# Kernel optimization log

Measured on AMD Instinct MI355X. Metric: run time of the kernel, lower is better.

Reference implementation:

```python
import jax, jax.numpy as jnp
import numpy as np

MASK_VALUE = 0.0
MAX_PATCHES = 7
MASK_MODES = ['courtain', 'center', 'border', 'patches']
B, C, H, W = 64, 3, 512, 512


def _build_mask(rng):
    # Faithful host-side replication of RandomMask's per-sample mask generation.
    mask = np.zeros((B, 1, H, W), dtype=np.float32)
    for i in range(B):
        mode = rng.choice(MASK_MODES)
        if mode == 'courtain':
            edge = rng.choice(['left', 'right', 'top', 'bottom'])
            pct = rng.uniform(0.1, 0.7)
            if edge == 'left':
                mask[i, :, :int(pct * H)] = 1
            elif edge == 'right':
                mask[i, :, int(pct * H):] = 1
            elif edge == 'top':
                mask[i, :, :, :int(pct * W)] = 1
            else:  # bottom
                mask[i, :, :, int(pct * W):] = 1
        elif mode in ('center', 'border'):
            pad_w = int(rng.uniform(0.1, 0.5) * H)
            pad_h = int(rng.uniform(0.1, 0.5) * W)
            mask[i, :, pad_w:-pad_w, pad_h:-pad_h] = 1
            if mode == 'border':
                mask[i] = 1 - mask[i]
        elif mode == 'patches':
            # NOTE: the original torch code indexes mask[i, :, py:py+sy, px:px+sx]
            # without assigning, so 'patches' is a no-op: mask stays zero. We
            # faithfully reproduce that (still draw the random numbers to keep
            # the RNG stream shape similar, though values are unused).
            num_patches = rng.integers(1, MAX_PATCHES + 1)
            for _ in range(num_patches):
                _ = rng.uniform(0.01, 0.9); _ = rng.uniform(0.01, 0.9)
                _ = rng.uniform(0, 0.99); _ = rng.uniform(0, 0.99)
    return mask


def setup_inputs() -> dict:
    key = jax.random.key(0)
    x = jax.random.normal(key, (B, C, H, W), dtype=jnp.float32)
    mask = jnp.asarray(_build_mask(np.random.default_rng(0)))
    return {"x": x, "mask": mask}


def reference(x, mask):
    # Fused blend: x * (1 - mask) + mask * mask_value  (mask broadcasts over C).
    # append_mask=False, so no channel concat.
    return x * (1.0 - mask) + mask * MASK_VALUE
```

## Files before the change

### kernel.cpp

```cpp
#include <hip/hip_runtime.h>


#define HW   (512 * 512)
#define C_   3
#define B_   64
#define VPP  (HW / 4)

typedef float fvec4 __attribute__((ext_vector_type(4)));

__global__ __launch_bounds__(256) void random_mask_blend(
    const fvec4* __restrict__ x,
    const fvec4* __restrict__ mask,
    fvec4* __restrict__ out)
{
    const int v = blockIdx.x * blockDim.x + threadIdx.x;
    const int b = blockIdx.y;

    const fvec4 mv = __builtin_nontemporal_load(&mask[(long long)b * VPP + v]);
    const long long base = ((long long)b * C_) * VPP + v;

    if (mv.x + mv.y + mv.z + mv.w == 4.0f) {
        const fvec4 z = {0.0f, 0.0f, 0.0f, 0.0f};
#pragma unroll
        for (int c = 0; c < C_; ++c)
            __builtin_nontemporal_store(z, &out[base + (long long)c * VPP]);
    } else {
        const fvec4 w = 1.0f - mv;
#pragma unroll
        for (int c = 0; c < C_; ++c) {
            const long long idx = base + (long long)c * VPP;
            const fvec4 xv = __builtin_nontemporal_load(&x[idx]);
            __builtin_nontemporal_store(xv * w, &out[idx]);
        }
    }
}

extern "C" void kernel_launch(void* const* d_in, const int* in_sizes, int n_in,
                              void* d_out, int out_size, void* d_ws, size_t ws_size,
                              hipStream_t stream) {
    const fvec4* x    = (const fvec4*)d_in[0];
    const fvec4* mask = (const fvec4*)d_in[1];
    fvec4* out        = (fvec4*)d_out;

    dim3 grid(VPP / 256, B_);
    dim3 block(256);
    random_mask_blend<<<grid, block, 0, stream>>>(x, mask, out);
}
```

Measured before the change: 337.1 us.

## Use persistent grid with per-thread batch loop and prefetched mask loads

Replaces the 2D grid of one-vector-per-thread blocks with a fixed 2048-block grid where each thread walks 8 batch samples at stride 8. The mask for the next sample is loaded ahead of the current one to overlap latency. This cuts block launch and scheduling overhead, but fewer waves in flight may reduce memory-level parallelism on a bandwidth-bound kernel.

```diff
diff --git a/kernel.cpp b/kernel.cpp
--- a/kernel.cpp
+++ b/kernel.cpp
@@ -5,6 +5,8 @@
 #define C_   3
 #define B_   64
 #define VPP  (HW / 4)
+#define NTHR (2048 * 256)
+#define CH   ((B_ * VPP) / NTHR)
 
 typedef float fvec4 __attribute__((ext_vector_type(4)));
 
@@ -13,24 +15,37 @@
     const fvec4* __restrict__ mask,
     fvec4* __restrict__ out)
 {
-    const int v = blockIdx.x * blockDim.x + threadIdx.x;
-    const int b = blockIdx.y;
+    const int g  = blockIdx.x * 256 + threadIdx.x;
+    const int v  = g & (VPP - 1);
+    const int b0 = g >> 16;
 
-    const fvec4 mv = __builtin_nontemporal_load(&mask[(long long)b * VPP + v]);
-    const long long base = ((long long)b * C_) * VPP + v;
+    fvec4 m_next = __builtin_nontemporal_load(
+        &mask[(long long)b0 * VPP + v]);
 
-    if (mv.x + mv.y + mv.z + mv.w == 4.0f) {
-        const fvec4 z = {0.0f, 0.0f, 0.0f, 0.0f};
 #pragma unroll
-        for (int c = 0; c < C_; ++c)
-            __builtin_nontemporal_store(z, &out[base + (long long)c * VPP]);
-    } else {
-        const fvec4 w = 1.0f - mv;
+    for (int c = 0; c < CH; ++c) {
+        const fvec4 m = m_next;
+        if (c + 1 < CH) {
+            m_next = __builtin_nontemporal_load(
+                &mask[(long long)((c + 1) * 8 + b0) * VPP + v]);
+        }
+
+        const int b = c * 8 + b0;
+        const long long base = ((long long)b * C_) * VPP + v;
+
+        if (m.x + m.y + m.z + m.w == 4.0f) {
+            const fvec4 z = {0.0f, 0.0f, 0.0f, 0.0f};
 #pragma unroll
-        for (int c = 0; c < C_; ++c) {
-            const long long idx = base + (long long)c * VPP;
-            const fvec4 xv = __builtin_nontemporal_load(&x[idx]);
-            __builtin_nontemporal_store(xv * w, &out[idx]);
+            for (int ch = 0; ch < C_; ++ch)
+                __builtin_nontemporal_store(z, &out[base + (long long)ch * VPP]);
+        } else {
+            const fvec4 w = 1.0f - m;
+#pragma unroll
+            for (int ch = 0; ch < C_; ++ch) {
+                const long long idx = base + (long long)ch * VPP;
+                const fvec4 xv = __builtin_nontemporal_load(&x[idx]);
+                __builtin_nontemporal_store(xv * w, &out[idx]);
+            }
         }
     }
 }
@@ -42,7 +57,7 @@
     const fvec4* mask = (const fvec4*)d_in[1];
     fvec4* out        = (fvec4*)d_out;
 
-    dim3 grid(VPP / 256, B_);
+    dim3 grid(2048);
     dim3 block(256);
     random_mask_blend<<<grid, block, 0, stream>>>(x, mask, out);
 }
```

New measurement: 343.2 us. No clear change (+1.8%).
